# Optimization experiments

Measured on AMD Instinct MI355X. Metric: run time of the kernel, lower is better.

## Reference

```python
import jax, jax.numpy as jnp
import numpy as np

B, N, D, C, H = 16384, 32, 256, 128, 8
LEAKY_ALPHA = 0.2  # tf.nn.leaky_relu default


def setup_inputs() -> dict:
    key = jax.random.key(0)
    k1, k2, k3, k4 = jax.random.split(key, 4)
    return {
        "node_feats": jax.random.normal(k1, (B, D), dtype=jnp.float32),
        "neighbors_feats": jax.random.normal(k2, (B, N, D), dtype=jnp.float32),
        "kernel": jax.random.normal(k3, (D, C), dtype=jnp.float32) * 0.05,
        "attn_kernel": jax.random.normal(k4, (1, H, 2 * C), dtype=jnp.float32) * 0.05,
        "attn_bias": jnp.zeros((H * C,), dtype=jnp.float32),
    }


def reference(node_feats, neighbors_feats, kernel, attn_kernel, attn_bias):
    # Project node and neighbor features: [B,C], [B,N,C]
    node_p = jnp.einsum('bd,dc->bc', node_feats, kernel)
    neigh_p = jnp.einsum('bnd,dc->bnc', neighbors_feats, kernel)
    # attn_kernel [1,H,2C]: split instead of materializing tile+concat [B,N,2C]
    a = attn_kernel[0]                 # [H, 2C]
    a_src, a_dst = a[:, :C], a[:, C:]  # each [H, C]
    # score[b,n,h] = concat(node_p[b], neigh_p[b,n]) . a[h]
    scores = (jnp.einsum('bc,hc->bh', node_p, a_src)[:, None, :]
              + jnp.einsum('bnc,hc->bnh', neigh_p, a_dst))  # [B,N,H]
    scores = jnp.transpose(scores, (0, 2, 1))  # [B,H,N]
    coef = jax.nn.softmax(jax.nn.leaky_relu(scores, LEAKY_ALPHA), axis=-1)
    # dropout is identity at inference (Keras default training=False)
    z = jnp.einsum('bhn,bnc->bhc', coef, neigh_p)  # [B,H,C]
    z = z.reshape(B, H * C) + attn_bias            # concat heads + bias
    return z[None, ...]  # [1,B,H*C]
```

## Files before the change

kernel.cpp:

```cpp
#include <hip/hip_runtime.h>

#define BB 16384
#define NN 32
#define DD 256
#define CC 128
#define HH 8
#define LDSTR 260
#define ALPHA 0.2f

__global__ __launch_bounds__(256) void ka_kernel(const float* __restrict__ kern,
                                                 const float* __restrict__ attn,
                                                 float* __restrict__ KaT) {
    int i = blockIdx.x * 256 + threadIdx.x;
    int which = i >> 11;
    int r = i & 2047;
    int h = r >> 8;
    int d = r & 255;
    const float* krow = kern + d * CC;
    const float* arow = attn + h * (2 * CC) + which * CC;
    float s = 0.f;
#pragma unroll 8
    for (int c = 0; c < CC; ++c) s += krow[c] * arow[c];
    KaT[i] = s;
}

__global__ __launch_bounds__(256) void gat_kernel(const float* __restrict__ node,
                                                  const float* __restrict__ neigh,
                                                  const float* __restrict__ kern,
                                                  const float* __restrict__ bias,
                                                  const float* __restrict__ KaT,
                                                  float* __restrict__ out) {
    const int b = blockIdx.x;
    const int t = threadIdx.x;

    __shared__ __align__(16) float smem[13248];
    float* sNeigh   = smem;
    float* sKas     = smem + 8320;
    float* sAgg     = smem + 8320;
    float* sKad     = smem + 10400;
    float* sNode    = smem + 12480;
    float* sScores  = smem + 12736;
    float* sCoef    = smem + 12992;

    const float4* nb4 = (const float4*)(neigh) + (size_t)b * (NN * DD / 4);
#pragma unroll
    for (int k = 0; k < 8; ++k) {
        int j  = k * 256 + t;
        int n  = j >> 6;
        int d4 = j & 63;
        ((float4*)(sNeigh + n * LDSTR))[d4] = nb4[j];
    }
    const float4* ka4 = (const float4*)KaT;
#pragma unroll
    for (int k = 0; k < 2; ++k) {
        int j4 = k * 256 + t;
        int h  = j4 >> 6;
        int d4 = j4 & 63;
        ((float4*)(sKas + h * LDSTR))[d4] = ka4[j4];
        ((float4*)(sKad + h * LDSTR))[d4] = ka4[512 + j4];
    }
    sNode[t] = node[(size_t)b * DD + t];
    __syncthreads();

    {
        int n = t >> 3, h = t & 7;
        const float4* nr = (const float4*)(sNeigh + n * LDSTR);
        const float4* kd = (const float4*)(sKad + h * LDSTR);
        const float4* ks = (const float4*)(sKas + h * LDSTR);
        const float4* nd = (const float4*)sNode;
        float s = 0.f;
#pragma unroll 8
        for (int d4 = 0; d4 < 64; ++d4) {
            float4 a = nr[d4], w = kd[d4], c = nd[d4], e = ks[d4];
            s += a.x * w.x + a.y * w.y + a.z * w.z + a.w * w.w;
            s += c.x * e.x + c.y * e.y + c.z * e.z + c.w * e.w;
        }
        s = (s > 0.f) ? s : ALPHA * s;
        sScores[n * 8 + h] = s;
    }
    __syncthreads();

    {
        int n = t >> 3, h = t & 7;
        float m = -1e30f;
#pragma unroll
        for (int j = 0; j < NN; ++j) m = fmaxf(m, sScores[j * 8 + h]);
        float denom = 0.f;
#pragma unroll
        for (int j = 0; j < NN; ++j) denom += __expf(sScores[j * 8 + h] - m);
        float e = __expf(sScores[n * 8 + h] - m);
        sCoef[h * 32 + n] = e / denom;
    }
    __syncthreads();

    {
        float acc[8] = {0.f, 0.f, 0.f, 0.f, 0.f, 0.f, 0.f, 0.f};
#pragma unroll 8
        for (int n = 0; n < NN; ++n) {
            float v = sNeigh[n * LDSTR + t];
#pragma unroll
            for (int h = 0; h < HH; ++h) acc[h] += sCoef[h * 32 + n] * v;
        }
#pragma unroll
        for (int h = 0; h < HH; ++h) sAgg[h * 256 + t] = acc[h];
    }
    __syncthreads();

    {
        int c = t & 127;
        int g = t >> 7;
        float acc[8] = {0.f, 0.f, 0.f, 0.f, 0.f, 0.f, 0.f, 0.f};
        int dbase = g * 128;
#pragma unroll 2
        for (int d4 = 0; d4 < 32; ++d4) {
            int d = dbase + d4 * 4;
            float kv0 = kern[(size_t)(d + 0) * CC + c];
            float kv1 = kern[(size_t)(d + 1) * CC + c];
            float kv2 = kern[(size_t)(d + 2) * CC + c];
            float kv3 = kern[(size_t)(d + 3) * CC + c];
#pragma unroll
            for (int h = 0; h < HH; ++h) {
                float4 ag = ((const float4*)(sAgg + h * 256))[g * 32 + d4];
                acc[h] += ag.x * kv0 + ag.y * kv1 + ag.z * kv2 + ag.w * kv3;
            }
        }
        float* sP = sNeigh;
#pragma unroll
        for (int h = 0; h < HH; ++h) sP[g * 1024 + h * 128 + c] = acc[h];
    }
    __syncthreads();

    {
        const float4* sP4   = (const float4*)sNeigh;
        const float4* bias4 = (const float4*)bias;
        float4 p0 = sP4[t];
        float4 p1 = sP4[256 + t];
        float4 bv = bias4[t];
        float4 r;
        r.x = p0.x + p1.x + bv.x;
        r.y = p0.y + p1.y + bv.y;
        r.z = p0.z + p1.z + bv.z;
        r.w = p0.w + p1.w + bv.w;
        ((float4*)(out + (size_t)b * (HH * CC)))[t] = r;
    }
}

extern "C" void kernel_launch(void* const* d_in, const int* in_sizes, int n_in,
                              void* d_out, int out_size, void* d_ws, size_t ws_size,
                              hipStream_t stream) {
    const float* node  = (const float*)d_in[0];
    const float* neigh = (const float*)d_in[1];
    const float* kern  = (const float*)d_in[2];
    const float* attn  = (const float*)d_in[3];
    const float* bias  = (const float*)d_in[4];
    float* out = (float*)d_out;
    float* KaT = (float*)d_ws;

    hipLaunchKernelGGL(ka_kernel, dim3(16), dim3(256), 0, stream, kern, attn, KaT);
    hipLaunchKernelGGL(gat_kernel, dim3(BB), dim3(256), 0, stream,
                       node, neigh, kern, bias, KaT, out);
}
```

Baseline: 949.6 us.

## Rewrite GAT kernel with bf16 MFMA for projection, scores and aggregation

```diff
diff --git a/kernel.cpp b/kernel.cpp
--- a/kernel.cpp
+++ b/kernel.cpp
@@ -5,143 +5,192 @@
 #define DD 256
 #define CC 128
 #define HH 8
-#define LDSTR 260
 #define ALPHA 0.2f
 
-__global__ __launch_bounds__(256) void ka_kernel(const float* __restrict__ kern,
-                                                 const float* __restrict__ attn,
-                                                 float* __restrict__ KaT) {
-    int i = blockIdx.x * 256 + threadIdx.x;
-    int which = i >> 11;
-    int r = i & 2047;
-    int h = r >> 8;
-    int d = r & 255;
-    const float* krow = kern + d * CC;
-    const float* arow = attn + h * (2 * CC) + which * CC;
-    float s = 0.f;
-#pragma unroll 8
-    for (int c = 0; c < CC; ++c) s += krow[c] * arow[c];
-    KaT[i] = s;
-}
-
-__global__ __launch_bounds__(256) void gat_kernel(const float* __restrict__ node,
-                                                  const float* __restrict__ neigh,
-                                                  const float* __restrict__ kern,
-                                                  const float* __restrict__ bias,
-                                                  const float* __restrict__ KaT,
-                                                  float* __restrict__ out) {
-    const int b = blockIdx.x;
-    const int t = threadIdx.x;
-
-    __shared__ __align__(16) float smem[13248];
-    float* sNeigh   = smem;
-    float* sKas     = smem + 8320;
-    float* sAgg     = smem + 8320;
-    float* sKad     = smem + 10400;
-    float* sNode    = smem + 12480;
-    float* sScores  = smem + 12736;
-    float* sCoef    = smem + 12992;
-
-    const float4* nb4 = (const float4*)(neigh) + (size_t)b * (NN * DD / 4);
-#pragma unroll
-    for (int k = 0; k < 8; ++k) {
-        int j  = k * 256 + t;
-        int n  = j >> 6;
-        int d4 = j & 63;
-        ((float4*)(sNeigh + n * LDSTR))[d4] = nb4[j];
-    }
-    const float4* ka4 = (const float4*)KaT;
-#pragma unroll
-    for (int k = 0; k < 2; ++k) {
-        int j4 = k * 256 + t;
-        int h  = j4 >> 6;
-        int d4 = j4 & 63;
-        ((float4*)(sKas + h * LDSTR))[d4] = ka4[j4];
-        ((float4*)(sKad + h * LDSTR))[d4] = ka4[512 + j4];
-    }
-    sNode[t] = node[(size_t)b * DD + t];
+#define SA_STRIDE 264
+#define SP_STRIDE 48
+
+typedef __attribute__((ext_vector_type(8))) short bf16x8;
+typedef __attribute__((ext_vector_type(4))) float f32x4;
+
+__device__ __forceinline__ unsigned short f2b(float x) {
+    unsigned int u = __float_as_uint(x);
+    return (unsigned short)((u + 0x7fffu + ((u >> 16) & 1u)) >> 16);
+}
+__device__ __forceinline__ uint2 pack4(float a, float b, float c, float d) {
+    uint2 r;
+    r.x = (unsigned)f2b(a) | ((unsigned)f2b(b) << 16);
+    r.y = (unsigned)f2b(c) | ((unsigned)f2b(d) << 16);
+    return r;
+}
+
+__global__ __launch_bounds__(256) void prep_kernel(const float* __restrict__ kern,
+                                                   const float* __restrict__ attn,
+                                                   unsigned short* __restrict__ kfrag,
+                                                   unsigned short* __restrict__ sfrag) {
+    if (blockIdx.x < 16) {
+        int tid = blockIdx.x * 256 + threadIdx.x;
+        int nt   = tid >> 9;
+        int ks   = (tid >> 6) & 7;
+        int lane = tid & 63;
+        int q    = lane >> 4;
+        int cc   = lane & 15;
+        int c    = nt * 16 + cc;
+        unsigned short v[8];
+#pragma unroll
+        for (int j = 0; j < 8; ++j) {
+            int k = ks * 32 + q * 8 + j;
+            v[j] = f2b(kern[k * CC + c]);
+        }
+        uint4* dst = (uint4*)(kfrag + ((size_t)(nt * 8 + ks) * 64 + lane) * 8);
+        uint4 pk;
+        pk.x = (unsigned)v[0] | ((unsigned)v[1] << 16);
+        pk.y = (unsigned)v[2] | ((unsigned)v[3] << 16);
+        pk.z = (unsigned)v[4] | ((unsigned)v[5] << 16);
+        pk.w = (unsigned)v[6] | ((unsigned)v[7] << 16);
+        *dst = pk;
+    } else {
+        int sid = (blockIdx.x - 16) * 256 + threadIdx.x;
+        int ks   = sid >> 6;
+        int lane = sid & 63;
+        int q    = lane >> 4;
+        int cc   = lane & 15;
+        unsigned short v[8];
+#pragma unroll
+        for (int j = 0; j < 8; ++j) {
+            int k = ks * 32 + q * 8 + j;
+            const float* krow = kern + (size_t)k * CC;
+            const float* arow = (cc < 8) ? (attn + cc * (2 * CC) + CC)
+                                         : (attn + (cc - 8) * (2 * CC));
+            float s0 = 0.f, s1 = 0.f;
+#pragma unroll 4
+            for (int c = 0; c < CC; c += 2) {
+                s0 += krow[c] * arow[c];
+                s1 += krow[c + 1] * arow[c + 1];
+            }
+            v[j] = f2b(s0 + s1);
+        }
+        uint4* dst = (uint4*)(sfrag + ((size_t)ks * 64 + lane) * 8);
+        uint4 pk;
+        pk.x = (unsigned)v[0] | ((unsigned)v[1] << 16);
+        pk.y = (unsigned)v[2] | ((unsigned)v[3] << 16);
+        pk.z = (unsigned)v[4] | ((unsigned)v[5] << 16);
+        pk.w = (unsigned)v[6] | ((unsigned)v[7] << 16);
+        *dst = pk;
+    }
+}
+
+__global__ __launch_bounds__(256, 4) void gat_kernel(const float* __restrict__ node,
+                                                     const float* __restrict__ neigh,
+                                                     const float* __restrict__ bias,
+                                                     const unsigned short* __restrict__ kfrag,
+                                                     const unsigned short* __restrict__ sfrag,
+                                                     float* __restrict__ out) {
+    const int b    = blockIdx.x;
+    const int t    = threadIdx.x;
+    const int lane = t & 63;
+    const int wave = t >> 6;
+    const int q    = lane >> 4;
+    const int m15  = lane & 15;
+
+    __shared__ __align__(16) char smem[39712];
+    unsigned short* sA    = (unsigned short*)smem;
+    unsigned short* sP    = (unsigned short*)(smem + 25344);
+    unsigned short* cfrag = (unsigned short*)(smem + 37632);
+    float*          sDst  = (float*)(smem + 38656);
+    float*          sSrc  = (float*)(smem + 39680);
+
+    {
+        const float4* nb4 = (const float4*)(neigh + (size_t)b * (NN * DD));
+        const float4* nd4 = (const float4*)(node + (size_t)b * DD);
+        for (int j = t; j < 33 * 64; j += 256) {
+            int row = j >> 6, d4 = j & 63;
+            float4 v = (row < 32) ? nb4[row * 64 + d4] : nd4[d4];
+            *(uint2*)(sA + row * SA_STRIDE + d4 * 4) = pack4(v.x, v.y, v.z, v.w);
+        }
+    }
     __syncthreads();
 
+    if (wave < 3) {
+        const int mt = wave;
+        f32x4 acc = {0.f, 0.f, 0.f, 0.f};
+        const unsigned short* abase = sA + (mt * 16 + m15) * SA_STRIDE + q * 8;
+#pragma unroll
+        for (int ks = 0; ks < 8; ++ks) {
+            bf16x8 bfr = *(const bf16x8*)(sfrag + ((size_t)ks * 64 + lane) * 8);
+            bf16x8 afr = *(const bf16x8*)(abase + ks * 32);
+            acc = __builtin_amdgcn_mfma_f32_16x16x32_bf16(afr, bfr, acc, 0, 0, 0);
+        }
+#pragma unroll
+        for (int r = 0; r < 4; ++r) {
+            int row = mt * 16 + q * 4 + r;
+            if (row < 32 && m15 < 8) sDst[row * 8 + m15] = acc[r];
+            if (row == 32 && m15 >= 8) sSrc[m15 - 8] = acc[r];
+        }
+    }
+
+#pragma unroll
+    for (int nti = 0; nti < 2; ++nti) {
+        const int nt = wave * 2 + nti;
+        bf16x8 kb[8];
+#pragma unroll
+        for (int ks = 0; ks < 8; ++ks)
+            kb[ks] = *(const bf16x8*)(kfrag + ((size_t)(nt * 8 + ks) * 64 + lane) * 8);
+#pragma unroll
+        for (int mt = 0; mt < 2; ++mt) {
+            f32x4 acc = {0.f, 0.f, 0.f, 0.f};
+            const unsigned short* abase = sA + (mt * 16 + m15) * SA_STRIDE + q * 8;
+#pragma unroll
+            for (int ks = 0; ks < 8; ++ks) {
+                bf16x8 afr = *(const bf16x8*)(abase + ks * 32);
+                acc = __builtin_amdgcn_mfma_f32_16x16x32_bf16(afr, kb[ks], acc, 0, 0, 0);
+            }
+            int c  = nt * 16 + m15;
+            int n0 = mt * 16 + q * 4;
+            *(uint2*)(sP + c * SP_STRIDE + n0) = pack4(acc[0], acc[1], acc[2], acc[3]);
+        }
+    }
+    __syncthreads();
+
     {
-        int n = t >> 3, h = t & 7;
-        const float4* nr = (const float4*)(sNeigh + n * LDSTR);
-        const float4* kd = (const float4*)(sKad + h * LDSTR);
-        const float4* ks = (const float4*)(sKas + h * LDSTR);
-        const float4* nd = (const float4*)sNode;
-        float s = 0.f;
-#pragma unroll 8
-        for (int d4 = 0; d4 < 64; ++d4) {
-            float4 a = nr[d4], w = kd[d4], c = nd[d4], e = ks[d4];
-            s += a.x * w.x + a.y * w.y + a.z * w.z + a.w * w.w;
-            s += c.x * e.x + c.y * e.y + c.z * e.z + c.w * e.w;
-        }
-        s = (s > 0.f) ? s : ALPHA * s;
-        sScores[n * 8 + h] = s;
+        int h = t >> 5, n = t & 31;
+        float sc = sSrc[h] + sDst[n * 8 + h];
+        sc = fmaxf(sc, ALPHA * sc);
+        float m = sc;
+#pragma unroll
+        for (int off = 16; off >= 1; off >>= 1) m = fmaxf(m, __shfl_xor(m, off, 32));
+        float e = expf(sc - m);
+        float den = e;
+#pragma unroll
+        for (int off = 16; off >= 1; off >>= 1) den += __shfl_xor(den, off, 32);
+        float coef = e / den;
+        int l1 = (n >> 3) * 16 + h;
+        int jj = n & 7;
+        cfrag[l1 * 8 + jj] = f2b(coef);
+        cfrag[(l1 + 8) * 8 + jj] = 0;
     }
     __syncthreads();
 
     {
-        int n = t >> 3, h = t & 7;
-        float m = -1e30f;
-#pragma unroll
-        for (int j = 0; j < NN; ++j) m = fmaxf(m, sScores[j * 8 + h]);
-        float denom = 0.f;
-#pragma unroll
-        for (int j = 0; j < NN; ++j) denom += __expf(sScores[j * 8 + h] - m);
-        float e = __expf(sScores[n * 8 + h] - m);
-        sCoef[h * 32 + n] = e / denom;
-    }
-    __syncthreads();
-
-    {
-        float acc[8] = {0.f, 0.f, 0.f, 0.f, 0.f, 0.f, 0.f, 0.f};
-#pragma unroll 8
-        for (int n = 0; n < NN; ++n) {
-            float v = sNeigh[n * LDSTR + t];
-#pragma unroll
-            for (int h = 0; h < HH; ++h) acc[h] += sCoef[h * 32 + n] * v;
-        }
-#pragma unroll
-        for (int h = 0; h < HH; ++h) sAgg[h * 256 + t] = acc[h];
-    }
-    __syncthreads();
-
-    {
-        int c = t & 127;
-        int g = t >> 7;
-        float acc[8] = {0.f, 0.f, 0.f, 0.f, 0.f, 0.f, 0.f, 0.f};
-        int dbase = g * 128;
-#pragma unroll 2
-        for (int d4 = 0; d4 < 32; ++d4) {
-            int d = dbase + d4 * 4;
-            float kv0 = kern[(size_t)(d + 0) * CC + c];
-            float kv1 = kern[(size_t)(d + 1) * CC + c];
-            float kv2 = kern[(size_t)(d + 2) * CC + c];
-            float kv3 = kern[(size_t)(d + 3) * CC + c];
-#pragma unroll
-            for (int h = 0; h < HH; ++h) {
-                float4 ag = ((const float4*)(sAgg + h * 256))[g * 32 + d4];
-                acc[h] += ag.x * kv0 + ag.y * kv1 + ag.z * kv2 + ag.w * kv3;
+        bf16x8 cb = *(const bf16x8*)(cfrag + (size_t)lane * 8);
+        f32x4 zero = {0.f, 0.f, 0.f, 0.f};
+#pragma unroll
+        for (int i = 0; i < 2; ++i) {
+            int mt5 = wave * 2 + i;
+            bf16x8 afr = *(const bf16x8*)(sP + (mt5 * 16 + m15) * SP_STRIDE + q * 8);
+            f32x4 acc = __builtin_amdgcn_mfma_f32_16x16x32_bf16(afr, cb, zero, 0, 0, 0);
+            if (m15 < 8) {
+                int h  = m15;
+                int c0 = mt5 * 16 + q * 4;
+                float4 bv = *(const float4*)(bias + h * CC + c0);
+                float4 r;
+                r.x = acc[0] + bv.x;
+                r.y = acc[1] + bv.y;
+                r.z = acc[2] + bv.z;
+                r.w = acc[3] + bv.w;
+                *(float4*)(out + (size_t)b * (HH * CC) + h * CC + c0) = r;
             }
         }
-        float* sP = sNeigh;
-#pragma unroll
-        for (int h = 0; h < HH; ++h) sP[g * 1024 + h * 128 + c] = acc[h];
-    }
-    __syncthreads();
-
-    {
-        const float4* sP4   = (const float4*)sNeigh;
-        const float4* bias4 = (const float4*)bias;
-        float4 p0 = sP4[t];
-        float4 p1 = sP4[256 + t];
-        float4 bv = bias4[t];
-        float4 r;
-        r.x = p0.x + p1.x + bv.x;
-        r.y = p0.y + p1.y + bv.y;
-        r.z = p0.z + p1.z + bv.z;
-        r.w = p0.w + p1.w + bv.w;
-        ((float4*)(out + (size_t)b * (HH * CC)))[t] = r;
     }
 }
 
@@ -154,9 +203,11 @@
     const float* attn  = (const float*)d_in[3];
     const float* bias  = (const float*)d_in[4];
     float* out = (float*)d_out;
-    float* KaT = (float*)d_ws;
-
-    hipLaunchKernelGGL(ka_kernel, dim3(16), dim3(256), 0, stream, kern, attn, KaT);
+
+    unsigned short* kfrag = (unsigned short*)d_ws;
+    unsigned short* sfrag = (unsigned short*)((char*)d_ws + 65536);
+
+    hipLaunchKernelGGL(prep_kernel, dim3(18), dim3(256), 0, stream, kern, attn, kfrag, sfrag);
     hipLaunchKernelGGL(gat_kernel, dim3(BB), dim3(256), 0, stream,
-                       node, neigh, kern, bias, KaT, out);
-}
+                       node, neigh, bias, kfrag, sfrag, out);
+}
```

Result: faster. 793.4 us (-16.5%).
